# Kernel tuning notes

Hardware: AMD Instinct MI355X
Metric: run time of the kernel (lower is better)

The kernel has to match this reference:

```python
import itertools
import jax, jax.numpy as jnp
import numpy as np

B, RES = 256, 16
DIM, KEY_DIM, NUM_HEADS, ATTN_RATIO = 448, 32, 8, 4
SEQ = RES * RES
EXP_KEY_DIM = ATTN_RATIO * KEY_DIM          # 128
TOTAL_KEY = KEY_DIM * NUM_HEADS             # 256
TOTAL_EXP = EXP_KEY_DIM * NUM_HEADS         # 1024
QKV_DIM = TOTAL_EXP + 2 * TOTAL_KEY         # 1536
SCALE = KEY_DIM ** -0.5


def _build_bias_idxs():
    # Replicates the itertools.product loop from build()
    points = list(itertools.product(range(RES), range(RES)))
    offsets = {}
    idxs = []
    for p1 in points:
        for p2 in points:
            off = (abs(p1[0] - p2[0]), abs(p1[1] - p2[1]))
            if off not in offsets:
                offsets[off] = len(offsets)
            idxs.append(offsets[off])
    return np.asarray(idxs, dtype=np.int32).reshape(SEQ, SEQ), len(offsets)


def setup_inputs() -> dict:
    key = jax.random.key(0)
    ks = jax.random.split(key, 6)
    bias_idxs_np, n_off = _build_bias_idxs()
    std = 0.02
    return {
        "hidden_states": jax.random.normal(ks[0], (B, SEQ, DIM), dtype=jnp.float32),
        "qkv_w": jax.random.normal(ks[1], (DIM, QKV_DIM), dtype=jnp.float32) * std,
        "qkv_b": jnp.zeros((QKV_DIM,), dtype=jnp.float32),
        "proj_w": jax.random.normal(ks[2], (TOTAL_EXP, DIM), dtype=jnp.float32) * std,
        "proj_b": jnp.zeros((DIM,), dtype=jnp.float32),
        "attention_biases": jax.random.normal(ks[3], (NUM_HEADS, n_off), dtype=jnp.float32) * std,
        "attention_bias_idxs": jnp.asarray(bias_idxs_np),
    }


def reference(hidden_states, qkv_w, qkv_b, proj_w, proj_b, attention_biases, attention_bias_idxs):
    b, s, _ = hidden_states.shape
    qkv = hidden_states @ qkv_w + qkv_b                       # [B,S,1536]
    qkv = qkv.reshape(b, s, NUM_HEADS, KEY_DIM * 2 + EXP_KEY_DIM)
    q, k, v = jnp.split(qkv, [KEY_DIM, 2 * KEY_DIM], axis=3)  # [B,S,H,dk],[B,S,H,dk],[B,S,H,dv]
    scores = jnp.einsum("bqhd,bkhd->bhqk", q, k) * SCALE      # [B,H,S,S]
    bias = attention_biases[:, attention_bias_idxs]           # [H,S,S] gather
    probs = jax.nn.softmax(scores + bias[None], axis=-1)
    ctx = jnp.einsum("bhqk,bkhd->bqhd", probs, v)             # [B,S,H,dv]
    ctx = ctx.reshape(b, s, TOTAL_EXP)
    return ctx @ proj_w + proj_b
```

## Files before the change

kernel.cpp:

```cpp
#include <hip/hip_runtime.h>
#include <hip/hip_bf16.h>
#include <stdint.h>


typedef __attribute__((ext_vector_type(4))) float f32x4;
typedef __attribute__((ext_vector_type(8))) short short8;
typedef __attribute__((ext_vector_type(4))) unsigned short u16x4;

#define DEVINL static __device__ __forceinline__

DEVINL unsigned short f2bf(float f) {
  unsigned u = __float_as_uint(f);
  return (unsigned short)((u + 0x7FFFu + ((u >> 16) & 1u)) >> 16);
}
DEVINL float bf2f(short s) {
  return __uint_as_float(((unsigned)(unsigned short)s) << 16);
}

DEVINL void gload_lds16(const void* g, void* l) {
  __builtin_amdgcn_global_load_lds((const __attribute__((address_space(1))) void*)g,
                                   (__attribute__((address_space(3))) void*)l,
                                   16, 0, 0);
}

#define SCALE 0.17677669529663687f

#define WS_XB     ((size_t)0)
#define WS_CTX    ((size_t)0)
#define WS_WQT    ((size_t)134217728)
#define WS_WPT    ((size_t)135593984)
#define WS_QW     ((size_t)136642560)
#define WS_KW     ((size_t)170196992)
#define WS_VT     ((size_t)203751424)
#define WS_QKVBP  ((size_t)342163456)

DEVINL int qkv_perm(int np, float* sc) {
  *sc = 1.0f;
  if (np < 512) {
    const int h = np >> 6, c = np & 63;
    if (c < 32) *sc = SCALE;
    return h * 192 + c;
  }
  const int h = (np - 512) >> 7, e = (np - 512) & 127;
  return h * 192 + 64 + e;
}


__global__ void k_convert_x(const float* __restrict__ x, short* __restrict__ xb) {
  const size_t i = (size_t)blockIdx.x * blockDim.x + threadIdx.x;
  const f32x4* src = (const f32x4*)x + i * 2;
  f32x4 a = src[0], b = src[1];
  short8 o;
#pragma unroll
  for (int t = 0; t < 4; ++t) o[t] = (short)f2bf(a[t]);
#pragma unroll
  for (int t = 0; t < 4; ++t) o[4 + t] = (short)f2bf(b[t]);
  ((short8*)xb)[i] = o;
}

__global__ void k_prep_qkvw(const float* __restrict__ w, short* __restrict__ out) {
  const int idx = blockIdx.x * blockDim.x + threadIdx.x;
  if (idx >= 1536 * 448) return;
  const int np = idx / 448, k = idx - np * 448;
  float sc;
  const int n = qkv_perm(np, &sc);
  out[idx] = (short)f2bf(w[(size_t)k * 1536 + n] * sc);
}

__global__ void k_prep_qkvb(const float* __restrict__ bsrc, float* __restrict__ bdst) {
  const int np = blockIdx.x * blockDim.x + threadIdx.x;
  if (np >= 1536) return;
  float sc;
  const int n = qkv_perm(np, &sc);
  bdst[np] = bsrc[n] * sc;
}

__global__ void k_transpose_bf16(const float* __restrict__ in, short* __restrict__ out,
                                 int K, int N, int total) {
  const int idx = blockIdx.x * blockDim.x + threadIdx.x;
  if (idx >= total) return;
  const int n = idx / K, k = idx - n * K;
  const float v = (n < N) ? in[(size_t)k * N + n] : 0.0f;
  out[idx] = (short)f2bf(v);
}


template <int KSTEPS, int LDA, int LDB, bool SWAP>
DEVINL void gemm128_pipe(const short* __restrict__ A, const short* __restrict__ B,
                         short* Asm, short* Bsm, int m0, int n0, int tid,
                         f32x4 acc[4][4]) {
  const int lane = tid & 63, wave = tid >> 6;
  const int l15 = lane & 15, g = lane >> 4;
  const int wm = wave >> 1, wn = wave & 1;
  const int r8 = lane >> 3;
  const int scol = (((lane & 7) ^ r8) << 3);
  const int wbase = wave * 32;

  const short* Ab = A + (size_t)(m0 + wbase + r8) * LDA + scol;
  const short* Bb = B + (size_t)(n0 + wbase + r8) * LDB + scol;

#pragma unroll
  for (int c = 0; c < 4; ++c) {
    gload_lds16(Ab + (size_t)(c * 8) * LDA, Asm + (wbase + c * 8) * 64);
    gload_lds16(Bb + (size_t)(c * 8) * LDB, Bsm + (wbase + c * 8) * 64);
  }
  __syncthreads();

  for (int ks = 0; ks < KSTEPS; ++ks) {
    const int cur = ks & 1, nxt = cur ^ 1;
    if (ks + 1 < KSTEPS) {
      const int k0 = (ks + 1) * 64;
#pragma unroll
      for (int c = 0; c < 4; ++c) {
        gload_lds16(Ab + (size_t)(c * 8) * LDA + k0, Asm + nxt * 8192 + (wbase + c * 8) * 64);
        gload_lds16(Bb + (size_t)(c * 8) * LDB + k0, Bsm + nxt * 8192 + (wbase + c * 8) * 64);
      }
    }
#pragma unroll
    for (int s = 0; s < 2; ++s) {
      const int rslot = (((s * 4 + g) ^ (l15 & 7)) << 3);
      short8 a[4], b[4];
#pragma unroll
      for (int i = 0; i < 4; ++i)
        a[i] = *(const short8*)(Asm + cur * 8192 + (wm * 64 + i * 16 + l15) * 64 + rslot);
#pragma unroll
      for (int j = 0; j < 4; ++j)
        b[j] = *(const short8*)(Bsm + cur * 8192 + (wn * 64 + j * 16 + l15) * 64 + rslot);
#pragma unroll
      for (int i = 0; i < 4; ++i)
#pragma unroll
        for (int j = 0; j < 4; ++j)
          acc[i][j] = SWAP
              ? __builtin_amdgcn_mfma_f32_16x16x32_bf16(b[j], a[i], acc[i][j], 0, 0, 0)
              : __builtin_amdgcn_mfma_f32_16x16x32_bf16(a[i], b[j], acc[i][j], 0, 0, 0);
    }
    __syncthreads();
  }
}


union QkvSmem {
  struct { short a[2 * 8192]; short b[2 * 8192]; } ab;
  short tile[128 * 136];
};

__global__ __launch_bounds__(256) void k_qkv_gemm(
    const short* __restrict__ Xb, const short* __restrict__ Wt,
    const float* __restrict__ qkvbp,
    short* __restrict__ Qw, short* __restrict__ Kw, short* __restrict__ Vt) {
  __shared__ __align__(16) QkvSmem sm;
  const int tid = threadIdx.x;
  const int l = (blockIdx.x & 7) * 768 + (blockIdx.x >> 3);
  const int mt = l / 12, by = l - mt * 12;
  const int m0 = mt * 128, n0 = by * 128;

  const int lane = tid & 63, wave = tid >> 6;
  const int l15 = lane & 15, g = lane >> 4;
  const int wm = wave >> 1, wn = wave & 1;
  const int b0 = m0 >> 8, s0 = m0 & 255;

  f32x4 acc[4][4];
#pragma unroll
  for (int i = 0; i < 4; ++i)
#pragma unroll
    for (int j = 0; j < 4; ++j) acc[i][j] = (f32x4){0.f, 0.f, 0.f, 0.f};

  if (by >= 4) {
    gemm128_pipe<7, 448, 448, false>(Xb, Wt, sm.ab.a, sm.ab.b, m0, n0, tid, acc);
#pragma unroll
    for (int i = 0; i < 4; ++i) {
#pragma unroll
      for (int j = 0; j < 4; ++j) {
        const float bv = qkvbp[n0 + wn * 64 + j * 16 + l15];
        u16x4 pk;
#pragma unroll
        for (int r = 0; r < 4; ++r) pk[r] = f2bf(acc[i][j][r] + bv);
        *(u16x4*)&sm.tile[(wn * 64 + j * 16 + l15) * 136 + wm * 64 + i * 16 + g * 4] = pk;
      }
    }
    __syncthreads();
    const int bh = b0 * 8 + (by - 4);
#pragma unroll
    for (int p = 0; p < 8; ++p) {
      const int er = p * 16 + (tid >> 4);
      const int sc = (tid & 15) * 8;
      short8 v = *(const short8*)&sm.tile[er * 136 + sc];
      *(short8*)(Vt + (size_t)bh * 33792 + er * 264 + s0 + sc) = v;
    }
  } else {
    gemm128_pipe<7, 448, 448, true>(Xb, Wt, sm.ab.a, sm.ab.b, m0, n0, tid, acc);
#pragma unroll
    for (int i = 0; i < 4; ++i) {
      const int s = s0 + wm * 64 + i * 16 + l15;
#pragma unroll
      for (int j = 0; j < 4; ++j) {
        const int nbase = n0 + wn * 64 + j * 16 + g * 4;
        const f32x4 bv4 = *(const f32x4*)(qkvbp + nbase);
        u16x4 pk;
#pragma unroll
        for (int r = 0; r < 4; ++r) pk[r] = f2bf(acc[i][j][r] + bv4[r]);
        const int h = (nbase >> 6) & 7, c = nbase & 63;
        const int bh = b0 * 8 + (by << 1) + (nbase >> 6 & 1);
        short* dst = (c < 32) ? (Qw + ((size_t)bh * 256 + s) * 32 + c)
                              : (Kw + ((size_t)bh * 256 + s) * 32 + (c - 32));
        *(u16x4*)dst = pk;
        (void)h;
      }
    }
  }
}


__global__ __launch_bounds__(512, 4) void k_attn(
    const short* __restrict__ Qw, const short* __restrict__ Kw,
    const short* __restrict__ Vt, const float* __restrict__ attb, int n_off,
    short* __restrict__ CTX) {
  __shared__ short Ps[4][32 * 264];
  __shared__ float rinv[4][32];
  __shared__ float bias_sm[256];

  const int tid = threadIdx.x, lane = tid & 63, wave = tid >> 6;
  const int l15 = lane & 15, g = lane >> 4;
  const int bh = blockIdx.x;
  const int b = bh >> 3, h = bh & 7;

  if (tid < 256) bias_sm[tid] = attb[h * n_off + tid];
  __syncthreads();

  const short* Qb = Qw + (size_t)bh * 8192;
  const short* Kb = Kw + (size_t)bh * 8192;
  const short* Vb = Vt + (size_t)bh * 33792;

  for (int ph = 0; ph < 2; ++ph) {
    const int Q0 = ph * 128;

    {
      short8 aq[4][2];
#pragma unroll
      for (int u = 0; u < 4; ++u)
#pragma unroll
        for (int i = 0; i < 2; ++i)
          aq[u][i] = *(const short8*)(Qb + (Q0 + u * 32 + i * 16 + l15) * 32 + g * 8);

#pragma unroll
      for (int fj = 0; fj < 2; ++fj) {
        const int kk0 = wave * 32 + fj * 16;
        const short8 bk = *(const short8*)(Kb + (kk0 + l15) * 32 + g * 8);
        const int kk = kk0 + l15;
        const int kr = kk >> 4, kc = kk & 15;
#pragma unroll
        for (int u = 0; u < 4; ++u) {
#pragma unroll
          for (int i = 0; i < 2; ++i) {
            const int q0 = Q0 + u * 32 + i * 16;
            f32x4 acc;
#pragma unroll
            for (int r = 0; r < 4; ++r) {
              const int qrow = q0 + g * 4 + r;
              const int qr = qrow >> 4, qc = qrow & 15;
              const int a = (qr > kr) ? qr - kr : kr - qr;
              const int bo = (qc > kc) ? qc - kc : kc - qc;
              acc[r] = bias_sm[a * 16 + bo];
            }
            acc = __builtin_amdgcn_mfma_f32_16x16x32_bf16(aq[u][i], bk, acc, 0, 0, 0);
#pragma unroll
            for (int r = 0; r < 4; ++r)
              Ps[u][(i * 16 + g * 4 + r) * 264 + kk] = (short)f2bf(acc[r]);
          }
        }
      }
    }
    __syncthreads();

    {
      const int r = tid >> 4, part = tid & 15;
#pragma unroll
      for (int u = 0; u < 4; ++u) {
        short* rowp = &Ps[u][r * 264 + part * 16];
        short8 x0 = ((const short8*)rowp)[0];
        short8 x1 = ((const short8*)rowp)[1];
        float v[16];
#pragma unroll
        for (int t = 0; t < 8; ++t) { v[t] = bf2f(x0[t]); v[8 + t] = bf2f(x1[t]); }
        float mx = v[0];
#pragma unroll
        for (int t = 1; t < 16; ++t) mx = fmaxf(mx, v[t]);
#pragma unroll
        for (int d = 1; d < 16; d <<= 1) mx = fmaxf(mx, __shfl_xor(mx, d));
        float sum = 0.f;
#pragma unroll
        for (int t = 0; t < 16; ++t) { v[t] = __expf(v[t] - mx); sum += v[t]; }
#pragma unroll
        for (int d = 1; d < 16; d <<= 1) sum += __shfl_xor(sum, d);
        short8 o0, o1;
#pragma unroll
        for (int t = 0; t < 8; ++t) { o0[t] = (short)f2bf(v[t]); o1[t] = (short)f2bf(v[8 + t]); }
        ((short8*)rowp)[0] = o0;
        ((short8*)rowp)[1] = o1;
        if (part == 0) rinv[u][r] = 1.0f / sum;
      }
    }
    __syncthreads();

    {
      f32x4 cacc[4][2];
#pragma unroll
      for (int u = 0; u < 4; ++u)
#pragma unroll
        for (int qt = 0; qt < 2; ++qt) cacc[u][qt] = (f32x4){0.f, 0.f, 0.f, 0.f};

      const int e = wave * 16 + l15;
#pragma unroll
      for (int ks = 0; ks < 8; ++ks) {
        const short8 bv = *(const short8*)(Vb + e * 264 + ks * 32 + g * 8);
#pragma unroll
        for (int u = 0; u < 4; ++u)
#pragma unroll
          for (int qt = 0; qt < 2; ++qt) {
            const short8 ap = *(const short8*)&Ps[u][(qt * 16 + l15) * 264 + ks * 32 + g * 8];
            cacc[u][qt] = __builtin_amdgcn_mfma_f32_16x16x32_bf16(ap, bv, cacc[u][qt], 0, 0, 0);
          }
      }

#pragma unroll
      for (int u = 0; u < 4; ++u)
#pragma unroll
        for (int qt = 0; qt < 2; ++qt) {
          const int qb = qt * 16 + g * 4;
#pragma unroll
          for (int r = 0; r < 4; ++r) {
            const int q = Q0 + u * 32 + qb + r;
            CTX[((size_t)b * 256 + q) * 1024 + h * 128 + wave * 16 + l15] =
                (short)f2bf(cacc[u][qt][r] * rinv[u][qb + r]);
          }
        }
    }
    __syncthreads();
  }
}


__global__ __launch_bounds__(256) void k_proj_gemm(
    const short* __restrict__ CTX, const short* __restrict__ Wpt,
    const float* __restrict__ projb, float* __restrict__ out) {
  __shared__ __align__(16) short Asm[2 * 8192];
  __shared__ __align__(16) short Bsm[2 * 8192];
  const int tid = threadIdx.x;
  const int l = (blockIdx.x & 7) * 256 + (blockIdx.x >> 3);
  const int mt = l >> 2, nt = l & 3;
  const int m0 = mt * 128, n0 = nt * 128;
  f32x4 acc[4][4];
#pragma unroll
  for (int i = 0; i < 4; ++i)
#pragma unroll
    for (int j = 0; j < 4; ++j) acc[i][j] = (f32x4){0.f, 0.f, 0.f, 0.f};

  gemm128_pipe<16, 1024, 1024, false>(CTX, Wpt, Asm, Bsm, m0, n0, tid, acc);

  const int lane = tid & 63, wave = tid >> 6;
  const int l15 = lane & 15, g = lane >> 4;
  const int wm = wave >> 1, wn = wave & 1;
#pragma unroll
  for (int i = 0; i < 4; ++i) {
    const int mb = m0 + wm * 64 + i * 16 + g * 4;
#pragma unroll
    for (int j = 0; j < 4; ++j) {
      const int n = n0 + wn * 64 + j * 16 + l15;
      if (n < 448) {
        const float bv = projb[n];
#pragma unroll
        for (int r = 0; r < 4; ++r)
          out[(size_t)(mb + r) * 448 + n] = acc[i][j][r] + bv;
      }
    }
  }
}


extern "C" void kernel_launch(void* const* d_in, const int* in_sizes, int n_in,
                              void* d_out, int out_size, void* d_ws, size_t ws_size,
                              hipStream_t stream) {
  const float* X      = (const float*)d_in[0];
  const float* qkv_w  = (const float*)d_in[1];
  const float* qkv_b  = (const float*)d_in[2];
  const float* proj_w = (const float*)d_in[3];
  const float* proj_b = (const float*)d_in[4];
  const float* att_b  = (const float*)d_in[5];
  const int n_off = in_sizes[5] / 8;

  char* ws = (char*)d_ws;
  short* Xb    = (short*)(ws + WS_XB);
  short* CTX   = (short*)(ws + WS_CTX);
  short* WQT   = (short*)(ws + WS_WQT);
  short* WPT   = (short*)(ws + WS_WPT);
  short* Qw    = (short*)(ws + WS_QW);
  short* Kw    = (short*)(ws + WS_KW);
  short* Vt    = (short*)(ws + WS_VT);
  float* QKVBP = (float*)(ws + WS_QKVBP);

  k_convert_x<<<14336, 256, 0, stream>>>(X, Xb);
  k_prep_qkvw<<<(1536 * 448 + 255) / 256, 256, 0, stream>>>(qkv_w, WQT);
  k_prep_qkvb<<<6, 256, 0, stream>>>(qkv_b, QKVBP);
  k_transpose_bf16<<<(512 * 1024 + 255) / 256, 256, 0, stream>>>(proj_w, WPT, 1024, 448, 512 * 1024);

  k_qkv_gemm<<<6144, 256, 0, stream>>>(Xb, WQT, QKVBP, Qw, Kw, Vt);
  k_attn<<<2048, 512, 0, stream>>>(Qw, Kw, Vt, att_b, n_off, CTX);
  k_proj_gemm<<<2048, 256, 0, stream>>>(CTX, WPT, proj_b, (float*)d_out);
}
```

Measured before the change: 391.7 us.

## Triple-buffer proj GEMM A tiles, fold log2e into scale, simplify bias indexing

```diff
diff --git a/kernel.cpp b/kernel.cpp
--- a/kernel.cpp
+++ b/kernel.cpp
@@ -24,6 +24,7 @@
 }
 
 #define SCALE 0.17677669529663687f
+#define LOG2E 1.4426950408889634f
 
 #define WS_XB     ((size_t)0)
 #define WS_CTX    ((size_t)0)
@@ -38,7 +39,7 @@
   *sc = 1.0f;
   if (np < 512) {
     const int h = np >> 6, c = np & 63;
-    if (c < 32) *sc = SCALE;
+    if (c < 32) *sc = SCALE * LOG2E;
     return h * 192 + c;
   }
   const int h = (np - 512) >> 7, e = (np - 512) & 127;
@@ -139,6 +140,81 @@
 }
 
 
+template <int KSTEPS, int LDA, int LDB>
+DEVINL void gemm128_pipe3(const short* __restrict__ A, const short* __restrict__ B,
+                          short* Asm , short* Bsm ,
+                          int m0, int n0, int tid, f32x4 acc[4][4]) {
+  const int lane = tid & 63, wave = tid >> 6;
+  const int l15 = lane & 15, g = lane >> 4;
+  const int wm = wave >> 1, wn = wave & 1;
+  const int r8 = lane >> 3;
+  const int scol = (((lane & 7) ^ r8) << 3);
+  const int wbase = wave * 32;
+
+  const short* Ab = A + (size_t)(m0 + wbase + r8) * LDA + scol;
+  const short* Bb = B + (size_t)(n0 + wbase + r8) * LDB + scol;
+
+  auto stageA = [&](int k) {
+    short* dst = Asm + (k % 3) * 8192 + wbase * 64;
+    const short* src = Ab + (size_t)k * 64;
+#pragma unroll
+    for (int c = 0; c < 4; ++c) gload_lds16(src + (size_t)(c * 8) * LDA, dst + c * 512);
+  };
+  auto stageB = [&](int k) {
+    short* dst = Bsm + (k % 2) * 8192 + wbase * 64;
+    const short* src = Bb + (size_t)k * 64;
+#pragma unroll
+    for (int c = 0; c < 4; ++c) gload_lds16(src + (size_t)(c * 8) * LDB, dst + c * 512);
+  };
+  auto compute = [&](int k) {
+    const short* Ac = Asm + (k % 3) * 8192;
+    const short* Bc = Bsm + (k % 2) * 8192;
+#pragma unroll
+    for (int s = 0; s < 2; ++s) {
+      const int rslot = (((s * 4 + g) ^ (l15 & 7)) << 3);
+      short8 a[4], b[4];
+#pragma unroll
+      for (int i = 0; i < 4; ++i)
+        a[i] = *(const short8*)(Ac + (wm * 64 + i * 16 + l15) * 64 + rslot);
+#pragma unroll
+      for (int j = 0; j < 4; ++j)
+        b[j] = *(const short8*)(Bc + (wn * 64 + j * 16 + l15) * 64 + rslot);
+#pragma unroll
+      for (int i = 0; i < 4; ++i)
+#pragma unroll
+        for (int j = 0; j < 4; ++j)
+          acc[i][j] = __builtin_amdgcn_mfma_f32_16x16x32_bf16(a[i], b[j], acc[i][j], 0, 0, 0);
+    }
+  };
+
+  stageB(0); stageA(0); stageA(1);
+  asm volatile("s_waitcnt vmcnt(4)" ::: "memory");
+  __builtin_amdgcn_s_barrier();
+  __builtin_amdgcn_sched_barrier(0);
+
+#pragma unroll
+  for (int ks = 0; ks < KSTEPS - 2; ++ks) {
+    stageB(ks + 1);
+    stageA(ks + 2);
+    asm volatile("s_waitcnt vmcnt(12)" ::: "memory");
+    __builtin_amdgcn_s_barrier();
+    __builtin_amdgcn_sched_barrier(0);
+    compute(ks);
+    __builtin_amdgcn_s_barrier();
+  }
+  stageB(KSTEPS - 1);
+  asm volatile("s_waitcnt vmcnt(8)" ::: "memory");
+  __builtin_amdgcn_s_barrier();
+  __builtin_amdgcn_sched_barrier(0);
+  compute(KSTEPS - 2);
+  __builtin_amdgcn_s_barrier();
+  asm volatile("s_waitcnt vmcnt(0)" ::: "memory");
+  __builtin_amdgcn_s_barrier();
+  __builtin_amdgcn_sched_barrier(0);
+  compute(KSTEPS - 1);
+}
+
+
 union QkvSmem {
   struct { short a[2 * 8192]; short b[2 * 8192]; } ab;
   short tile[128 * 136];
@@ -199,12 +275,11 @@
         u16x4 pk;
 #pragma unroll
         for (int r = 0; r < 4; ++r) pk[r] = f2bf(acc[i][j][r] + bv4[r]);
-        const int h = (nbase >> 6) & 7, c = nbase & 63;
+        const int c = nbase & 63;
         const int bh = b0 * 8 + (by << 1) + (nbase >> 6 & 1);
         short* dst = (c < 32) ? (Qw + ((size_t)bh * 256 + s) * 32 + c)
                               : (Kw + ((size_t)bh * 256 + s) * 32 + (c - 32));
         *(u16x4*)dst = pk;
-        (void)h;
       }
     }
   }
@@ -224,8 +299,15 @@
   const int bh = blockIdx.x;
   const int b = bh >> 3, h = bh & 7;
 
-  if (tid < 256) bias_sm[tid] = attb[h * n_off + tid];
+  if (tid < 256) bias_sm[tid] = attb[h * n_off + tid] * LOG2E;
   __syncthreads();
+
+  int offc[4];
+#pragma unroll
+  for (int r = 0; r < 4; ++r) {
+    const int d = g * 4 + r - l15;
+    offc[r] = (d < 0) ? -d : d;
+  }
 
   const short* Qb = Qw + (size_t)bh * 8192;
   const short* Kb = Kw + (size_t)bh * 8192;
@@ -247,21 +329,16 @@
         const int kk0 = wave * 32 + fj * 16;
         const short8 bk = *(const short8*)(Kb + (kk0 + l15) * 32 + g * 8);
         const int kk = kk0 + l15;
-        const int kr = kk >> 4, kc = kk & 15;
+        const int kr = wave * 2 + fj;
 #pragma unroll
         for (int u = 0; u < 4; ++u) {
 #pragma unroll
           for (int i = 0; i < 2; ++i) {
-            const int q0 = Q0 + u * 32 + i * 16;
+            const int qr = ph * 8 + u * 2 + i;
+            const int ab = ((qr > kr) ? qr - kr : kr - qr) << 4;
             f32x4 acc;
 #pragma unroll
-            for (int r = 0; r < 4; ++r) {
-              const int qrow = q0 + g * 4 + r;
-              const int qr = qrow >> 4, qc = qrow & 15;
-              const int a = (qr > kr) ? qr - kr : kr - qr;
-              const int bo = (qc > kc) ? qc - kc : kc - qc;
-              acc[r] = bias_sm[a * 16 + bo];
-            }
+            for (int r = 0; r < 4; ++r) acc[r] = bias_sm[ab + offc[r]];
             acc = __builtin_amdgcn_mfma_f32_16x16x32_bf16(aq[u][i], bk, acc, 0, 0, 0);
 #pragma unroll
             for (int r = 0; r < 4; ++r)
@@ -289,7 +366,7 @@
         for (int d = 1; d < 16; d <<= 1) mx = fmaxf(mx, __shfl_xor(mx, d));
         float sum = 0.f;
 #pragma unroll
-        for (int t = 0; t < 16; ++t) { v[t] = __expf(v[t] - mx); sum += v[t]; }
+        for (int t = 0; t < 16; ++t) { v[t] = exp2f(v[t] - mx); sum += v[t]; }
 #pragma unroll
         for (int d = 1; d < 16; d <<= 1) sum += __shfl_xor(sum, d);
         short8 o0, o1;
@@ -343,7 +420,7 @@
 __global__ __launch_bounds__(256) void k_proj_gemm(
     const short* __restrict__ CTX, const short* __restrict__ Wpt,
     const float* __restrict__ projb, float* __restrict__ out) {
-  __shared__ __align__(16) short Asm[2 * 8192];
+  __shared__ __align__(16) short Asm[3 * 8192];
   __shared__ __align__(16) short Bsm[2 * 8192];
   const int tid = threadIdx.x;
   const int l = (blockIdx.x & 7) * 256 + (blockIdx.x >> 3);
@@ -355,7 +432,7 @@
 #pragma unroll
     for (int j = 0; j < 4; ++j) acc[i][j] = (f32x4){0.f, 0.f, 0.f, 0.f};
 
-  gemm128_pipe<16, 1024, 1024, false>(CTX, Wpt, Asm, Bsm, m0, n0, tid, acc);
+  gemm128_pipe3<16, 1024, 1024>(CTX, Wpt, Asm, Bsm, m0, n0, tid, acc);
 
   const int lane = tid & 63, wave = tid >> 6;
   const int l15 = lane & 15, g = lane >> 4;
```

Result: no change. 389.0 us (-0.7%).
